# Kernel tuning notes

Measured on AMD Instinct MI355X. Metric: run time of the kernel, lower is better.

## Reference

```python
import jax, jax.numpy as jnp
import numpy as np

D_MODEL = 64  # per-head dim; temper = sqrt(D_MODEL)
NEG_INF = -1e30  # stand-in for -inf; safe under softmax and autodiff


def setup_inputs() -> dict:
    key = jax.random.key(0)
    kq, kk, kv, km = jax.random.split(key, 4)
    B, S, D = 16, 2048, 64
    q = jax.random.normal(kq, (B, S, D), dtype=jnp.float32)
    k = jax.random.normal(kk, (B, S, D), dtype=jnp.float32)
    v = jax.random.normal(kv, (B, S, D), dtype=jnp.float32)
    attn_mask = jax.random.bernoulli(km, 0.1, (B, S, S))
    return {"q": q, "k": k, "v": v, "attn_mask": attn_mask}


def reference(q, k, v, attn_mask):
    temper = jnp.sqrt(jnp.float32(D_MODEL))
    # [B, Sq, Sk] scores
    attn = jnp.einsum("bqd,bkd->bqk", q, k) / temper
    attn = jnp.where(attn_mask, NEG_INF, attn)
    attn = jax.nn.softmax(attn, axis=2)
    # dropout is identity in eval / attn_dropout=0.0
    output = jnp.einsum("bqk,bkd->bqd", attn, v)
    return (output, attn)
```

## Files before the change

### kernel.cpp

```cpp
#include <hip/hip_runtime.h>
#include <hip/hip_bf16.h>
#include <stdint.h>


#define S_DIM 2048
#define D_DIM 64

typedef short short8 __attribute__((ext_vector_type(8)));
typedef float floatx4 __attribute__((ext_vector_type(4)));
typedef unsigned short ushort8v __attribute__((ext_vector_type(8)));
typedef uint32_t u32a __attribute__((may_alias));

__device__ __forceinline__ unsigned short f2bf(float x) {
    uint32_t u = __float_as_uint(x);
    u += 0x7fffu + ((u >> 16) & 1u);
    return (unsigned short)(u >> 16);
}
__device__ __forceinline__ float bf2f(unsigned short h) {
    return __uint_as_float((uint32_t)h << 16);
}

__global__ __launch_bounds__(256) void prep_kv(
    const float* __restrict__ k,
    unsigned short* __restrict__ khi2, unsigned short* __restrict__ klo2,
    const float* __restrict__ v, unsigned short* __restrict__ vfrag)
{
    const int blk = blockIdx.x;
    const int tid = threadIdx.x;

    if (blk < 1024) {
        const int e  = blk;
        const int b  = e >> 6;
        const int kc = (e & 63) * 2 + (tid >> 7);
        const int t  = tid & 127;
        const int s = t >> 6, quad = (t >> 4) & 3, n16 = t & 15;
        const float* src = k + ((size_t)(b * S_DIM) + kc * 16 + n16) * D_DIM + s * 32 + quad * 8;
        float4 x0 = *(const float4*)src;
        float4 x1 = *(const float4*)(src + 4);
        float xs[8] = {x0.x, x0.y, x0.z, x0.w, x1.x, x1.y, x1.z, x1.w};
        ushort8v h, l;
        #pragma unroll
        for (int p = 0; p < 8; ++p) {
            unsigned short hp = f2bf(xs[p]);
            h[p] = hp;
            l[p] = f2bf(xs[p] - bf2f(hp));
        }
        size_t o = ((size_t)(b * 128 + kc)) * 1024 + (size_t)t * 8;
        *(ushort8v*)(khi2 + o) = h;
        *(ushort8v*)(klo2 + o) = l;
    } else {
        const int e  = blk - 1024;
        const int b  = e >> 6;
        const int kb = e & 63;
        const int nc = tid >> 6, quad = (tid >> 4) & 3, n16 = tid & 15;
        ushort8v o;
        #pragma unroll
        for (int p = 0; p < 8; ++p) {
            float x = v[((size_t)(b * S_DIM) + kb * 32 + quad * 8 + p) * D_DIM + nc * 16 + n16];
            o[p] = f2bf(x);
        }
        *(ushort8v*)(vfrag + ((size_t)(b * 64 + kb)) * 2048 + (size_t)tid * 8) = o;
    }
}

__global__ __launch_bounds__(1024) void attn_fused_v7(
    const float* __restrict__ q,
    const unsigned short* __restrict__ khi2, const unsigned short* __restrict__ klo2,
    const unsigned short* __restrict__ vfrag,
    const int* __restrict__ mask,
    float* __restrict__ out, float* __restrict__ attn)
{
    __shared__ __align__(16) float qlds[16 * 68];
    __shared__ __align__(16) unsigned short pbuf[16 * 16 * 36];
    __shared__ __align__(16) float obuf[8 * 16 * 68];
    __shared__ float mxtab[16 * 16];
    __shared__ float ltab[16 * 16];

    const int tid  = threadIdx.x;
    const int w    = tid >> 6;
    const int lane = tid & 63;
    const int quad = lane >> 4;
    const int n16  = lane & 15;
    const int wg   = blockIdx.x;
    const int swz  = (wg & 7) * 256 + (wg >> 3);
    const int b    = swz >> 7;
    const int q0   = (swz & 127) * 16;
    const int key0 = w * 128;

    int4 mx[8];
    {
        const int* mrow = mask + ((size_t)(b * S_DIM) + q0 + (lane >> 5)) * S_DIM
                               + key0 + (lane & 31) * 4;
        #pragma unroll
        for (int it = 0; it < 8; ++it)
            mx[it] = *(const int4*)(mrow + (size_t)(2 * it) * S_DIM);
    }

    {
        int m = tid >> 6, d = tid & 63;
        qlds[m * 68 + d] = q[((size_t)(b * S_DIM + q0 + m)) * D_DIM + d];
    }
    __syncthreads();

    short8 ahi[2], alo[2];
    #pragma unroll
    for (int s = 0; s < 2; ++s) {
        const float* qp = &qlds[n16 * 68 + s * 32 + quad * 8];
        union { unsigned short u[8]; short8 v; } H, L;
        #pragma unroll
        for (int p = 0; p < 8; ++p) {
            float x = qp[p];
            unsigned short hp = f2bf(x);
            H.u[p] = hp;
            L.u[p] = f2bf(x - bf2f(hp));
        }
        ahi[s] = H.v; alo[s] = L.v;
    }

    uint32_t kept = 0;
    {
        const int lr = lane >> 2;
        const int le = lane & 3;
        #pragma unroll
        for (int it = 0; it < 8; ++it) {
            #pragma unroll
            for (int e = 0; e < 4; ++e) {
                int val = (e == 0 ? mx[it].x : e == 1 ? mx[it].y
                         : e == 2 ? mx[it].z : mx[it].w);
                unsigned long long bal = __ballot(val != 0);
                if (lr == 2 * it && le == e)     kept = (uint32_t)bal;
                if (lr == 2 * it + 1 && le == e) kept = (uint32_t)(bal >> 32);
            }
        }
    }

    floatx4 sc[8];
    const unsigned short* khb = khi2 + (size_t)b * 131072;
    const unsigned short* klb = klo2 + (size_t)b * 131072;
    #pragma unroll
    for (int c = 0; c < 8; ++c) {
        const int kc = w * 8 + c;
        floatx4 acc = {0.f, 0.f, 0.f, 0.f};
        #pragma unroll
        for (int s = 0; s < 2; ++s) {
            const size_t off = (size_t)((kc * 2 + s) * 4 + quad) * 128 + n16 * 8;
            short8 BH = *(const short8*)(khb + off);
            short8 BL = *(const short8*)(klb + off);
            acc = __builtin_amdgcn_mfma_f32_16x16x32_bf16(ahi[s], BH, acc, 0, 0, 0);
            acc = __builtin_amdgcn_mfma_f32_16x16x32_bf16(ahi[s], BL, acc, 0, 0, 0);
            acc = __builtin_amdgcn_mfma_f32_16x16x32_bf16(alo[s], BH, acc, 0, 0, 0);
        }
        sc[c] = acc;
    }
    #pragma unroll
    for (int r = 0; r < 4; ++r) {
        int srcl = (quad * 4 + r) * 4 + (n16 & 3);
        uint32_t wd = (uint32_t)__shfl((int)kept, srcl, 64);
        #pragma unroll
        for (int c = 0; c < 8; ++c) {
            uint32_t bit = (wd >> (c * 4 + (n16 >> 2))) & 1u;
            sc[c][r] = bit ? -1e30f : sc[c][r] * 0.125f;
        }
    }

    #pragma unroll
    for (int r = 0; r < 4; ++r) {
        float mxv = sc[0][r];
        #pragma unroll
        for (int c = 1; c < 8; ++c) mxv = fmaxf(mxv, sc[c][r]);
        #pragma unroll
        for (int o = 1; o < 16; o <<= 1) mxv = fmaxf(mxv, __shfl_xor(mxv, o, 64));
        if (n16 == 0) mxtab[w * 16 + quad * 4 + r] = mxv;
    }
    __syncthreads();
    #pragma unroll
    for (int r = 0; r < 4; ++r) {
        float mf = -3e38f;
        #pragma unroll
        for (int w2 = 0; w2 < 16; ++w2) mf = fmaxf(mf, mxtab[w2 * 16 + quad * 4 + r]);
        float l = 0.f;
        #pragma unroll
        for (int c = 0; c < 8; ++c) {
            float e = __expf(sc[c][r] - mf);
            sc[c][r] = e;
            l += e;
        }
        #pragma unroll
        for (int o = 1; o < 16; o <<= 1) l += __shfl_xor(l, o, 64);
        if (n16 == 0) ltab[w * 16 + quad * 4 + r] = l;
    }
    __syncthreads();
    #pragma unroll
    for (int r = 0; r < 4; ++r) {
        float l = 0.f;
        #pragma unroll
        for (int w2 = 0; w2 < 16; ++w2) l += ltab[w2 * 16 + quad * 4 + r];
        float inv = 1.0f / l;
        #pragma unroll
        for (int c = 0; c < 8; ++c) sc[c][r] *= inv;
    }

    {
        float* arow = attn + (size_t)(b * S_DIM + q0 + quad * 4) * S_DIM + key0 + n16;
        #pragma unroll
        for (int c = 0; c < 8; ++c) {
            #pragma unroll
            for (int r = 0; r < 4; ++r) arow[(size_t)r * S_DIM + c * 16] = sc[c][r];
        }
    }

    floatx4 o0 = {0,0,0,0}, o1 = {0,0,0,0}, o2 = {0,0,0,0}, o3 = {0,0,0,0};
    unsigned short* pw = pbuf + w * 576;
    const unsigned short* vtb = vfrag + (size_t)b * 131072;
    #pragma unroll
    for (int s2 = 0; s2 < 4; ++s2) {
        #pragma unroll
        for (int h = 0; h < 2; ++h) {
            const int c = s2 * 2 + h;
            #pragma unroll
            for (int r = 0; r < 4; ++r)
                pw[(quad * 4 + r) * 36 + h * 16 + n16] = f2bf(sc[c][r]);
        }
        short8 pa;
        {
            const u32a* pr = (const u32a*)((const char*)pbuf +
                                   (size_t)w * 1152 + n16 * 72 + quad * 16);
            union { uint32_t u[4]; short8 v; } P;
            P.u[0] = pr[0]; P.u[1] = pr[1]; P.u[2] = pr[2]; P.u[3] = pr[3];
            pa = P.v;
        }
        const int kb = w * 4 + s2;
        #pragma unroll
        for (int nc = 0; nc < 4; ++nc) {
            const size_t off = (size_t)((kb * 4 + nc) * 4 + quad) * 128 + n16 * 8;
            short8 bv = *(const short8*)(vtb + off);
            floatx4& oo = (nc == 0 ? o0 : nc == 1 ? o1 : nc == 2 ? o2 : o3);
            oo = __builtin_amdgcn_mfma_f32_16x16x32_bf16(pa, bv, oo, 0, 0, 0);
        }
    }

    if (w < 8) {
        #pragma unroll
        for (int nc = 0; nc < 4; ++nc) {
            floatx4 oo = (nc == 0 ? o0 : nc == 1 ? o1 : nc == 2 ? o2 : o3);
            #pragma unroll
            for (int i = 0; i < 4; ++i)
                obuf[(w * 16 + quad * 4 + i) * 68 + nc * 16 + n16] = oo[i];
        }
    }
    __syncthreads();
    if (w >= 8) {
        #pragma unroll
        for (int nc = 0; nc < 4; ++nc) {
            floatx4 oo = (nc == 0 ? o0 : nc == 1 ? o1 : nc == 2 ? o2 : o3);
            #pragma unroll
            for (int i = 0; i < 4; ++i)
                obuf[((w - 8) * 16 + quad * 4 + i) * 68 + nc * 16 + n16] += oo[i];
        }
    }
    __syncthreads();
    {
        int m = tid >> 6, d = tid & 63;
        float a = 0.f;
        #pragma unroll
        for (int w2 = 0; w2 < 8; ++w2) a += obuf[(w2 * 16 + m) * 68 + d];
        out[(size_t)(b * S_DIM + q0 + m) * D_DIM + d] = a;
    }
}

__global__ __launch_bounds__(512) void attn_fused_v1(
    const float* __restrict__ q, const float* __restrict__ k,
    const float* __restrict__ v, const int* __restrict__ mask,
    float* __restrict__ out, float* __restrict__ attn)
{
    __shared__ __align__(16) float qlds[16 * 68];
    __shared__ __align__(16) unsigned short pbuf[8 * 16 * 36];
    __shared__ __align__(16) float obuf[8 * 16 * 68];
    __shared__ float mxtab[8 * 16];
    __shared__ float ltab[8 * 16];

    const int tid  = threadIdx.x;
    const int w    = tid >> 6;
    const int lane = tid & 63;
    const int quad = lane >> 4;
    const int n16  = lane & 15;
    const int b    = blockIdx.x >> 7;
    const int q0   = (blockIdx.x & 127) * 16;
    const int key0 = w * 256;

    {
        int m = tid >> 5, d = (tid & 31) * 2;
        float2 qv = *(const float2*)(q + ((size_t)(b * S_DIM + q0 + m)) * D_DIM + d);
        qlds[m * 68 + d]     = qv.x;
        qlds[m * 68 + d + 1] = qv.y;
    }
    __syncthreads();

    short8 ahi[2], alo[2];
    #pragma unroll
    for (int s = 0; s < 2; ++s) {
        const float* qp = &qlds[n16 * 68 + s * 32 + quad * 8];
        union { __hip_bfloat162 h[4]; short8 v; } H, L;
        #pragma unroll
        for (int p = 0; p < 4; ++p) {
            float x0 = qp[2 * p], x1 = qp[2 * p + 1];
            __hip_bfloat162 h2 = __float22bfloat162_rn(float2{x0, x1});
            float l0 = x0 - __bfloat162float(h2.x);
            float l1 = x1 - __bfloat162float(h2.y);
            H.h[p] = h2;
            L.h[p] = __float22bfloat162_rn(float2{l0, l1});
        }
        ahi[s] = H.v; alo[s] = L.v;
    }

    floatx4 sc[16];
    const size_t kvbase = (size_t)(b * S_DIM) * D_DIM;
    #pragma unroll
    for (int c = 0; c < 16; ++c) {
        const int key = key0 + c * 16 + n16;
        const int* mp = mask + (size_t)(b * S_DIM + q0 + quad * 4) * S_DIM + key;
        int mk0 = mp[0], mk1 = mp[S_DIM], mk2 = mp[2 * S_DIM], mk3 = mp[3 * S_DIM];
        floatx4 acc = {0.f, 0.f, 0.f, 0.f};
        #pragma unroll
        for (int s = 0; s < 2; ++s) {
            const float* kp = k + kvbase + (size_t)key * D_DIM + s * 32 + quad * 8;
            float4 k0 = *(const float4*)kp;
            float4 k1 = *(const float4*)(kp + 4);
            float kf[8] = {k0.x, k0.y, k0.z, k0.w, k1.x, k1.y, k1.z, k1.w};
            union { __hip_bfloat162 h[4]; short8 v; } BH, BL;
            #pragma unroll
            for (int p = 0; p < 4; ++p) {
                float x0 = kf[2 * p], x1 = kf[2 * p + 1];
                __hip_bfloat162 h2 = __float22bfloat162_rn(float2{x0, x1});
                BH.h[p] = h2;
                BL.h[p] = __float22bfloat162_rn(
                    float2{x0 - __bfloat162float(h2.x), x1 - __bfloat162float(h2.y)});
            }
            acc = __builtin_amdgcn_mfma_f32_16x16x32_bf16(ahi[s], BH.v, acc, 0, 0, 0);
            acc = __builtin_amdgcn_mfma_f32_16x16x32_bf16(ahi[s], BL.v, acc, 0, 0, 0);
            acc = __builtin_amdgcn_mfma_f32_16x16x32_bf16(alo[s], BH.v, acc, 0, 0, 0);
        }
        sc[c][0] = mk0 ? -1e30f : acc[0] * 0.125f;
        sc[c][1] = mk1 ? -1e30f : acc[1] * 0.125f;
        sc[c][2] = mk2 ? -1e30f : acc[2] * 0.125f;
        sc[c][3] = mk3 ? -1e30f : acc[3] * 0.125f;
    }

    #pragma unroll
    for (int r = 0; r < 4; ++r) {
        float mx = sc[0][r];
        #pragma unroll
        for (int c = 1; c < 16; ++c) mx = fmaxf(mx, sc[c][r]);
        #pragma unroll
        for (int o = 1; o < 16; o <<= 1) mx = fmaxf(mx, __shfl_xor(mx, o, 64));
        if (n16 == 0) mxtab[w * 16 + quad * 4 + r] = mx;
    }
    __syncthreads();
    #pragma unroll
    for (int r = 0; r < 4; ++r) {
        float mf = -3e38f;
        #pragma unroll
        for (int w2 = 0; w2 < 8; ++w2) mf = fmaxf(mf, mxtab[w2 * 16 + quad * 4 + r]);
        float l = 0.f;
        #pragma unroll
        for (int c = 0; c < 16; ++c) {
            float e = __expf(sc[c][r] - mf);
            sc[c][r] = e;
            l += e;
        }
        #pragma unroll
        for (int o = 1; o < 16; o <<= 1) l += __shfl_xor(l, o, 64);
        if (n16 == 0) ltab[w * 16 + quad * 4 + r] = l;
    }
    __syncthreads();
    #pragma unroll
    for (int r = 0; r < 4; ++r) {
        float l = 0.f;
        #pragma unroll
        for (int w2 = 0; w2 < 8; ++w2) l += ltab[w2 * 16 + quad * 4 + r];
        float inv = 1.0f / l;
        #pragma unroll
        for (int c = 0; c < 16; ++c) sc[c][r] *= inv;
    }

    {
        float* arow = attn + (size_t)(b * S_DIM + q0 + quad * 4) * S_DIM + key0 + n16;
        #pragma unroll
        for (int c = 0; c < 16; ++c) {
            #pragma unroll
            for (int r = 0; r < 4; ++r) arow[(size_t)r * S_DIM + c * 16] = sc[c][r];
        }
    }

    floatx4 o0 = {0,0,0,0}, o1 = {0,0,0,0}, o2 = {0,0,0,0}, o3 = {0,0,0,0};
    unsigned short* pw = pbuf + w * 576;
    #pragma unroll
    for (int s2 = 0; s2 < 8; ++s2) {
        #pragma unroll
        for (int h = 0; h < 2; ++h) {
            const int c = s2 * 2 + h;
            #pragma unroll
            for (int r = 0; r < 4; ++r)
                pw[(quad * 4 + r) * 36 + h * 16 + n16] = f2bf(sc[c][r]);
        }
        __syncthreads();
        short8 pa;
        {
            const uint32_t* pr = (const uint32_t*)((const char*)pbuf +
                                   (size_t)w * 1152 + n16 * 72 + quad * 16);
            union { uint32_t u[4]; short8 v; } P;
            P.u[0] = pr[0]; P.u[1] = pr[1]; P.u[2] = pr[2]; P.u[3] = pr[3];
            pa = P.v;
        }
        const size_t vrow0 = (size_t)(b * S_DIM + key0 + s2 * 32 + quad * 8) * D_DIM;
        #pragma unroll
        for (int nc = 0; nc < 4; ++nc) {
            const float* vp = v + vrow0 + nc * 16 + n16;
            union { __hip_bfloat162 h[4]; short8 v8; } BV;
            #pragma unroll
            for (int p = 0; p < 4; ++p) {
                float x0 = vp[(size_t)(2 * p) * D_DIM];
                float x1 = vp[(size_t)(2 * p + 1) * D_DIM];
                BV.h[p] = __float22bfloat162_rn(float2{x0, x1});
            }
            floatx4& oo = (nc == 0 ? o0 : nc == 1 ? o1 : nc == 2 ? o2 : o3);
            oo = __builtin_amdgcn_mfma_f32_16x16x32_bf16(pa, BV.v8, oo, 0, 0, 0);
        }
        __syncthreads();
    }

    #pragma unroll
    for (int nc = 0; nc < 4; ++nc) {
        floatx4 oo = (nc == 0 ? o0 : nc == 1 ? o1 : nc == 2 ? o2 : o3);
        #pragma unroll
        for (int i = 0; i < 4; ++i)
            obuf[(w * 16 + quad * 4 + i) * 68 + nc * 16 + n16] = oo[i];
    }
    __syncthreads();
    #pragma unroll
    for (int t2 = 0; t2 < 2; ++t2) {
        int idx = tid + t2 * 512;
        int m = idx >> 6, d = idx & 63;
        float a = 0.f;
        #pragma unroll
        for (int w2 = 0; w2 < 8; ++w2) a += obuf[(w2 * 16 + m) * 68 + d];
        out[(size_t)(b * S_DIM + q0 + m) * D_DIM + d] = a;
    }
}

extern "C" void kernel_launch(void* const* d_in, const int* in_sizes, int n_in,
                              void* d_out, int out_size, void* d_ws, size_t ws_size,
                              hipStream_t stream) {
    const float* q    = (const float*)d_in[0];
    const float* k    = (const float*)d_in[1];
    const float* v    = (const float*)d_in[2];
    const int*   mask = (const int*)d_in[3];

    float* out  = (float*)d_out;
    float* attn = out + (size_t)16 * S_DIM * D_DIM;

    const size_t NE = (size_t)16 * S_DIM * D_DIM;
    const size_t need = NE * 2 * 3;
    if (d_ws != nullptr && ws_size >= need) {
        unsigned short* khi2  = (unsigned short*)d_ws;
        unsigned short* klo2  = khi2 + NE;
        unsigned short* vfrag = klo2 + NE;
        prep_kv<<<dim3(2048), dim3(256), 0, stream>>>(k, khi2, klo2, v, vfrag);
        attn_fused_v7<<<dim3(2048), dim3(1024), 0, stream>>>(q, khi2, klo2, vfrag, mask, out, attn);
    } else {
        attn_fused_v1<<<dim3(2048), dim3(512), 0, stream>>>(q, k, v, mask, out, attn);
    }
}
```

Baseline: 556.0 us.

## Alias shared buffers into one union and hoist QK MFMA before mask ballot

Puts the Q staging, P buffer and output reduction buffer into one aliased shared-memory region, shrinking LDS per block so more blocks can be resident per CU. To make this safe, the output reduction now runs in four serialized rounds of four waves each, with extra barriers. The QK^T MFMA loop is moved ahead of the mask-ballot step so its global K loads can overlap with the ballot work. The cost is more __syncthreads and serialized LDS accumulation, and correctness now depends on the barriers separating each phase that reuses the region.

```diff
diff --git a/kernel.cpp b/kernel.cpp
--- a/kernel.cpp
+++ b/kernel.cpp
@@ -63,18 +63,19 @@
     }
 }
 
-__global__ __launch_bounds__(1024) void attn_fused_v7(
+__global__ __launch_bounds__(1024) void attn_fused_v8(
     const float* __restrict__ q,
     const unsigned short* __restrict__ khi2, const unsigned short* __restrict__ klo2,
     const unsigned short* __restrict__ vfrag,
     const int* __restrict__ mask,
     float* __restrict__ out, float* __restrict__ attn)
 {
-    __shared__ __align__(16) float qlds[16 * 68];
-    __shared__ __align__(16) unsigned short pbuf[16 * 16 * 36];
-    __shared__ __align__(16) float obuf[8 * 16 * 68];
+    __shared__ __align__(16) char uni[18432];
     __shared__ float mxtab[16 * 16];
     __shared__ float ltab[16 * 16];
+    float* qlds          = (float*)uni;
+    unsigned short* pbuf = (unsigned short*)uni;
+    float* obuf          = (float*)uni;
 
     const int tid  = threadIdx.x;
     const int w    = tid >> 6;
@@ -117,6 +118,25 @@
         ahi[s] = H.v; alo[s] = L.v;
     }
 
+    floatx4 sc[8];
+    const unsigned short* khb = khi2 + (size_t)b * 131072;
+    const unsigned short* klb = klo2 + (size_t)b * 131072;
+    #pragma unroll
+    for (int c = 0; c < 8; ++c) {
+        const int kc = w * 8 + c;
+        floatx4 acc = {0.f, 0.f, 0.f, 0.f};
+        #pragma unroll
+        for (int s = 0; s < 2; ++s) {
+            const size_t off = (size_t)((kc * 2 + s) * 4 + quad) * 128 + n16 * 8;
+            short8 BH = *(const short8*)(khb + off);
+            short8 BL = *(const short8*)(klb + off);
+            acc = __builtin_amdgcn_mfma_f32_16x16x32_bf16(ahi[s], BH, acc, 0, 0, 0);
+            acc = __builtin_amdgcn_mfma_f32_16x16x32_bf16(ahi[s], BL, acc, 0, 0, 0);
+            acc = __builtin_amdgcn_mfma_f32_16x16x32_bf16(alo[s], BH, acc, 0, 0, 0);
+        }
+        sc[c] = acc;
+    }
+
     uint32_t kept = 0;
     {
         const int lr = lane >> 2;
@@ -133,25 +153,6 @@
             }
         }
     }
-
-    floatx4 sc[8];
-    const unsigned short* khb = khi2 + (size_t)b * 131072;
-    const unsigned short* klb = klo2 + (size_t)b * 131072;
-    #pragma unroll
-    for (int c = 0; c < 8; ++c) {
-        const int kc = w * 8 + c;
-        floatx4 acc = {0.f, 0.f, 0.f, 0.f};
-        #pragma unroll
-        for (int s = 0; s < 2; ++s) {
-            const size_t off = (size_t)((kc * 2 + s) * 4 + quad) * 128 + n16 * 8;
-            short8 BH = *(const short8*)(khb + off);
-            short8 BL = *(const short8*)(klb + off);
-            acc = __builtin_amdgcn_mfma_f32_16x16x32_bf16(ahi[s], BH, acc, 0, 0, 0);
-            acc = __builtin_amdgcn_mfma_f32_16x16x32_bf16(ahi[s], BL, acc, 0, 0, 0);
-            acc = __builtin_amdgcn_mfma_f32_16x16x32_bf16(alo[s], BH, acc, 0, 0, 0);
-        }
-        sc[c] = acc;
-    }
     #pragma unroll
     for (int r = 0; r < 4; ++r) {
         int srcl = (quad * 4 + r) * 4 + (n16 & 3);
@@ -239,7 +240,8 @@
         }
     }
 
-    if (w < 8) {
+    __syncthreads();
+    if (w < 4) {
         #pragma unroll
         for (int nc = 0; nc < 4; ++nc) {
             floatx4 oo = (nc == 0 ? o0 : nc == 1 ? o1 : nc == 2 ? o2 : o3);
@@ -249,7 +251,17 @@
         }
     }
     __syncthreads();
-    if (w >= 8) {
+    if (w >= 4 && w < 8) {
+        #pragma unroll
+        for (int nc = 0; nc < 4; ++nc) {
+            floatx4 oo = (nc == 0 ? o0 : nc == 1 ? o1 : nc == 2 ? o2 : o3);
+            #pragma unroll
+            for (int i = 0; i < 4; ++i)
+                obuf[((w - 4) * 16 + quad * 4 + i) * 68 + nc * 16 + n16] += oo[i];
+        }
+    }
+    __syncthreads();
+    if (w >= 8 && w < 12) {
         #pragma unroll
         for (int nc = 0; nc < 4; ++nc) {
             floatx4 oo = (nc == 0 ? o0 : nc == 1 ? o1 : nc == 2 ? o2 : o3);
@@ -259,11 +271,20 @@
         }
     }
     __syncthreads();
+    if (w >= 12) {
+        #pragma unroll
+        for (int nc = 0; nc < 4; ++nc) {
+            floatx4 oo = (nc == 0 ? o0 : nc == 1 ? o1 : nc == 2 ? o2 : o3);
+            #pragma unroll
+            for (int i = 0; i < 4; ++i)
+                obuf[((w - 12) * 16 + quad * 4 + i) * 68 + nc * 16 + n16] += oo[i];
+        }
+    }
+    __syncthreads();
     {
         int m = tid >> 6, d = tid & 63;
-        float a = 0.f;
-        #pragma unroll
-        for (int w2 = 0; w2 < 8; ++w2) a += obuf[(w2 * 16 + m) * 68 + d];
+        float a = obuf[(m) * 68 + d] + obuf[(16 + m) * 68 + d]
+                + obuf[(32 + m) * 68 + d] + obuf[(48 + m) * 68 + d];
         out[(size_t)(b * S_DIM + q0 + m) * D_DIM + d] = a;
     }
 }
@@ -466,7 +487,7 @@
         unsigned short* klo2  = khi2 + NE;
         unsigned short* vfrag = klo2 + NE;
         prep_kv<<<dim3(2048), dim3(256), 0, stream>>>(k, khi2, klo2, v, vfrag);
-        attn_fused_v7<<<dim3(2048), dim3(1024), 0, stream>>>(q, khi2, klo2, vfrag, mask, out, attn);
+        attn_fused_v8<<<dim3(2048), dim3(1024), 0, stream>>>(q, khi2, klo2, vfrag, mask, out, attn);
     } else {
         attn_fused_v1<<<dim3(2048), dim3(512), 0, stream>>>(q, k, v, mask, out, attn);
     }
```

New measurement: 566.3 us. No clear change (+1.8%).
